# Performance work log

Measured on AMD Instinct MI355X. Metric: run time of the kernel, lower is better.

Reference implementation:

```python
import jax, jax.numpy as jnp
import numpy as np

V = 50257; E = 1024; H = 1024; L = 256; NL = 2; D = 10


def setup_inputs() -> dict:
    key = jax.random.key(0)
    ks = jax.random.split(key, 16)
    n = lambda k, s: jax.random.normal(k, s, dtype=jnp.float32)
    return {
        "input_tok": jax.random.randint(ks[0], (1, 1), 0, V),
        "h0": n(ks[1], (NL, 1, H)),
        "c0": n(ks[2], (NL, 1, H)),
        "h_s": n(ks[3], (L, 1, H)),
        "h_t_tilde": n(ks[4], (1, 1, H)),
        "emb": n(ks[5], (V, E)) * 0.02,
        "Wp": n(ks[6], (H, H)) * (H ** -0.5),
        "wdot": n(ks[7], (1, H)) * (H ** -0.5),
        "Wbil": n(ks[8], (1, H, H)) * (H ** -0.5),
        "Wcomb": n(ks[9], (H, 2 * H)) * ((2 * H) ** -0.5),
        "bcomb": jnp.zeros((H,), jnp.float32),
        "Wih0": n(ks[10], (4 * H, E + H)) * ((E + H) ** -0.5),
        "Whh0": n(ks[11], (4 * H, H)) * (H ** -0.5),
        "bih0": jnp.zeros((4 * H,), jnp.float32),
        "bhh0": jnp.zeros((4 * H,), jnp.float32),
        "Wih1": n(ks[12], (4 * H, H)) * (H ** -0.5),
        "Whh1": n(ks[13], (4 * H, H)) * (H ** -0.5),
        "bih1": jnp.zeros((4 * H,), jnp.float32),
        "bhh1": jnp.zeros((4 * H,), jnp.float32),
        "Wout": n(ks[14], (V, H)) * (H ** -0.5),
        "bout": jnp.zeros((V,), jnp.float32),
    }


def _lstm_cell(x, h, c, Wih, Whh, bih, bhh):
    # torch LSTM gate order: i, f, g, o
    g = x @ Wih.T + bih + h @ Whh.T + bhh
    i, f, gg, o = jnp.split(g, 4, axis=-1)
    c2 = jax.nn.sigmoid(f) * c + jax.nn.sigmoid(i) * jnp.tanh(gg)
    h2 = jax.nn.sigmoid(o) * jnp.tanh(c2)
    return h2, c2


def reference(input_tok, h0, c0, h_s, h_t_tilde, emb, Wp, wdot, Wbil, Wcomb, bcomb,
              Wih0, Whh0, bih0, bhh0, Wih1, Whh1, bih1, bhh1, Wout, bout):
    embedding = emb[input_tok]                                  # [1,1,E]
    x = jnp.concatenate((embedding, h_t_tilde), axis=-1)[0]     # [1,E+H]
    h1, c1 = _lstm_cell(x, h0[0], c0[0], Wih0, Whh0, bih0, bhh0)
    h2, c2 = _lstm_cell(h1, h0[1], c0[1], Wih1, Whh1, bih1, bhh1)
    h_new = jnp.stack((h1, h2)); c_new = jnp.stack((c1, c2))
    h_t = h2                                                    # [1,H]
    Ls = h_s.shape[0]
    p_t = Ls * jax.nn.sigmoid(jnp.tanh(h_t @ Wp.T) @ wdot.T).squeeze()  # scalar
    s = jnp.round(p_t).astype(jnp.int32)
    idx = jnp.arange(Ls)
    lo = jnp.maximum(s - D, 0); hi = jnp.minimum(s + D, Ls - 1)
    mask = (idx >= lo) & (idx <= hi)                            # [L] local window
    # bilinear score h_t^T W h_s over all positions; mask outside window
    score = jnp.einsum('bh,ohk,lbk->lbo', h_t, Wbil, h_s)       # [L,1,1]
    neg = jnp.finfo(score.dtype).min
    a = jax.nn.softmax(jnp.where(mask[:, None, None], score, neg), axis=0)
    # NOTE: original uses exp(+d^2/(D/2)^2) (no minus sign); replicated faithfully.
    expo = jnp.where(mask, ((idx.astype(jnp.float32) - p_t) ** 2) / ((D / 2) ** 2), 0.0)
    a_t = a * jnp.exp(expo)[:, None, None]                      # [L,1,1]
    win = (hi - lo + 1).astype(jnp.float32)
    context = jnp.sum(a_t * h_s, axis=0, keepdims=True) / win   # [1,1,H] (mean over window)
    cat = jnp.concatenate((context, h_t[None]), axis=-1)        # [1,1,2H]
    h_t_tilde_new = jnp.tanh(cat @ Wcomb.T + bcomb)             # [1,1,H]
    y = jax.nn.log_softmax(h_t_tilde_new @ Wout.T + bout, axis=-1)  # [1,1,V]
    return (y, h_new, c_new, h_t_tilde_new, a_t, p_t)
```

## Files before the change

### kernel.cpp

```cpp
#include <hip/hip_runtime.h>
#include <math.h>

#define V 50257
#define E 1024
#define HH 1024
#define LL 256

#define O_H  (V)
#define O_C  (V + 2*HH)
#define O_HT (V + 4*HH)
#define O_A  (V + 5*HH)
#define O_P  (V + 5*HH + LL)

#define W_T    0
#define W_V    1024
#define W_H1   2048
#define W_H2   3072
#define W_Z    4096
#define W_BM   54400
#define W_BS   55424

#define NW   4096
#define MAXR 13

__device__ __forceinline__ float sigmoidf_(float x) { return 1.f / (1.f + expf(-x)); }
__device__ __forceinline__ float dot4(float4 a, float4 b) {
    return a.x * b.x + a.y * b.y + a.z * b.z + a.w * b.w;
}

__device__ __forceinline__ float block_sum(float v, float* red) {
    int lane = threadIdx.x & 63, wv = threadIdx.x >> 6;
#pragma unroll
    for (int o = 32; o > 0; o >>= 1) v += __shfl_down(v, o, 64);
    __syncthreads();
    if (lane == 0) red[wv] = v;
    __syncthreads();
    return red[0] + red[1] + red[2] + red[3];
}

__global__ void k_lstm(const float* __restrict__ Wih, const float* __restrict__ Whh,
                       const float* __restrict__ bih, const float* __restrict__ bhh,
                       const float* __restrict__ xa_base, const int* __restrict__ tok,
                       const float* __restrict__ xb, int na, int nb,
                       const float* __restrict__ hprev, const float* __restrict__ cprev,
                       float* __restrict__ hout, float* __restrict__ cout,
                       float* __restrict__ hout2, float* __restrict__ zero_buf) {
    const int u = blockIdx.x;
    const int K = na + nb;
    const int K4 = K >> 2, na4 = na >> 2;
    if (zero_buf && threadIdx.x == 0) zero_buf[u] = 0.f;
    const float* xa = tok ? (xa_base + (size_t)tok[0] * na) : xa_base;
    const float4* xa4 = (const float4*)xa;
    const float4* xb4 = (const float4*)xb;
    const float4* r0 = (const float4*)(Wih + (size_t)u * K);
    const float4* r1 = (const float4*)(Wih + (size_t)(u + HH) * K);
    const float4* r2 = (const float4*)(Wih + (size_t)(u + 2*HH) * K);
    const float4* r3 = (const float4*)(Wih + (size_t)(u + 3*HH) * K);
    float a0 = 0, a1 = 0, a2 = 0, a3 = 0;
    for (int j = threadIdx.x; j < K4; j += 256) {
        float4 xv = (j < na4) ? xa4[j] : xb4[j - na4];
        a0 += dot4(r0[j], xv); a1 += dot4(r1[j], xv);
        a2 += dot4(r2[j], xv); a3 += dot4(r3[j], xv);
    }
    const float4* s0 = (const float4*)(Whh + (size_t)u * HH);
    const float4* s1 = (const float4*)(Whh + (size_t)(u + HH) * HH);
    const float4* s2 = (const float4*)(Whh + (size_t)(u + 2*HH) * HH);
    const float4* s3 = (const float4*)(Whh + (size_t)(u + 3*HH) * HH);
    const float4* hp4 = (const float4*)hprev;
    {
        int j = threadIdx.x;
        float4 hv = hp4[j];
        a0 += dot4(s0[j], hv); a1 += dot4(s1[j], hv);
        a2 += dot4(s2[j], hv); a3 += dot4(s3[j], hv);
    }
    int lane = threadIdx.x & 63, wv = threadIdx.x >> 6;
#pragma unroll
    for (int o = 32; o > 0; o >>= 1) {
        a0 += __shfl_down(a0, o, 64);
        a1 += __shfl_down(a1, o, 64);
        a2 += __shfl_down(a2, o, 64);
        a3 += __shfl_down(a3, o, 64);
    }
    __shared__ float sm[4][4];
    if (lane == 0) { sm[wv][0] = a0; sm[wv][1] = a1; sm[wv][2] = a2; sm[wv][3] = a3; }
    __syncthreads();
    if (threadIdx.x == 0) {
        float gi = sm[0][0]+sm[1][0]+sm[2][0]+sm[3][0] + bih[u]        + bhh[u];
        float gf = sm[0][1]+sm[1][1]+sm[2][1]+sm[3][1] + bih[u+HH]     + bhh[u+HH];
        float gg = sm[0][2]+sm[1][2]+sm[2][2]+sm[3][2] + bih[u+2*HH]   + bhh[u+2*HH];
        float go = sm[0][3]+sm[1][3]+sm[2][3]+sm[3][3] + bih[u+3*HH]   + bhh[u+3*HH];
        float c = sigmoidf_(gf) * cprev[u] + sigmoidf_(gi) * tanhf(gg);
        float h = sigmoidf_(go) * tanhf(c);
        hout[u] = h; cout[u] = c; hout2[u] = h;
    }
}

__global__ void k_ptv(const float* __restrict__ Wp, const float* __restrict__ Wbil,
                      const float* __restrict__ h2, float* __restrict__ t_out,
                      float* __restrict__ v_out) {
    __shared__ float red[4];
    if (blockIdx.x < HH) {
        int r = blockIdx.x;
        const float4* row = (const float4*)(Wp + (size_t)r * HH);
        const float4* h24 = (const float4*)h2;
        float acc = dot4(row[threadIdx.x], h24[threadIdx.x]);
        float tot = block_sum(acc, red);
        if (threadIdx.x == 0) t_out[r] = tanhf(tot);
    } else {
        int b = blockIdx.x - HH;
        int h0 = b * 32;
        int k4 = threadIdx.x;
        const float4* W4 = (const float4*)Wbil;
        float4 acc = make_float4(0.f, 0.f, 0.f, 0.f);
        for (int h = h0; h < h0 + 32; ++h) {
            float hv = h2[h];
            float4 w = W4[(size_t)h * 256 + k4];
            acc.x += hv * w.x; acc.y += hv * w.y;
            acc.z += hv * w.z; acc.w += hv * w.w;
        }
        atomicAdd(&v_out[k4 * 4 + 0], acc.x);
        atomicAdd(&v_out[k4 * 4 + 1], acc.y);
        atomicAdd(&v_out[k4 * 4 + 2], acc.z);
        atomicAdd(&v_out[k4 * 4 + 3], acc.w);
    }
}

__global__ void k_combattn(const float* __restrict__ wdot, const float* __restrict__ t,
                           const float* __restrict__ v, const float* __restrict__ hs,
                           const float* __restrict__ h2, const float* __restrict__ Wcomb,
                           const float* __restrict__ bcomb,
                           float* __restrict__ outv, float* __restrict__ outv2,
                           float* __restrict__ ato, float* __restrict__ pto) {
    const int u = blockIdx.x, tid = threadIdx.x;
    const int lane = tid & 63, wv = tid >> 6;
    __shared__ float red[4];
    __shared__ float ssc[32];
    __shared__ float sa[LL];
    float p;
    {
        const float4* w4 = (const float4*)wdot;
        const float4* t4 = (const float4*)t;
        float acc = dot4(w4[tid], t4[tid]);
        p = (float)LL * sigmoidf_(block_sum(acc, red));
    }
    if (u == 0 && tid == 0) pto[0] = p;
    const int si = (int)rintf(p);
    const int lo = max(si - 10, 0), hi = min(si + 10, LL - 1);
    const int W = hi - lo + 1;
    const float4* v4 = (const float4*)v;
    for (int l = lo + wv; l <= hi; l += 4) {
        const float4* row = (const float4*)(hs + (size_t)l * HH);
        float a = 0.f;
#pragma unroll
        for (int j = lane; j < 256; j += 64) a += dot4(row[j], v4[j]);
#pragma unroll
        for (int o = 32; o > 0; o >>= 1) a += __shfl_xor(a, o, 64);
        if (lane == 0) ssc[l - lo] = a;
    }
    __syncthreads();
    float M = -INFINITY;
    for (int i = 0; i < W; ++i) M = fmaxf(M, ssc[i]);
    float S = 0.f;
    for (int i = 0; i < W; ++i) S += expf(ssc[i] - M);
    {
        bool mask = (tid >= lo) && (tid <= hi);
        int wi = min(max(tid - lo, 0), 31);
        float e = mask ? expf(ssc[wi] - M) : 0.f;
        float d = (float)tid - p;
        float at = mask ? (e / S) * expf(d * d * 0.04f) : 0.f;
        sa[tid] = at;
        if (u == 0) ato[tid] = at;
    }
    __syncthreads();
    const float4* hs4 = (const float4*)hs;
    float4 c = make_float4(0.f, 0.f, 0.f, 0.f);
    for (int l = lo; l <= hi; ++l) {
        float a = sa[l];
        float4 hv = hs4[(size_t)l * 256 + tid];
        c.x += a * hv.x; c.y += a * hv.y; c.z += a * hv.z; c.w += a * hv.w;
    }
    const float inv_win = 1.f / (float)W;
    c.x *= inv_win; c.y *= inv_win; c.z *= inv_win; c.w *= inv_win;
    {
        const float4* row = (const float4*)(Wcomb + (size_t)u * (2 * HH));
        const float4* h24 = (const float4*)h2;
        float acc = dot4(row[tid], c) + dot4(row[256 + tid], h24[tid]);
        float tot = block_sum(acc, red);
        if (tid == 0) {
            float h = tanhf(tot + bcomb[u]);
            outv[u] = h; outv2[u] = h;
        }
    }
}

__global__ void k_logits(const float* __restrict__ Wout, const float* __restrict__ bout,
                         const float* __restrict__ x, float* __restrict__ z,
                         float* __restrict__ bmax, float* __restrict__ bsum) {
    const int tid = threadIdx.x, lane = tid & 63, wvi = tid >> 6;
    const int w = blockIdx.x * 4 + wvi;
    const float4* x4 = (const float4*)x;
    float4 x0 = x4[lane], x1 = x4[lane + 64], x2 = x4[lane + 128], x3 = x4[lane + 192];
    float m = -INFINITY, s = 0.f;
    for (int i = 0; i < MAXR; ++i) {
        int r = w + i * NW;
        if (r < V) {
            const float4* row = (const float4*)(Wout + (size_t)r * 1024) + lane;
            float acc = dot4(row[0], x0) + dot4(row[64], x1)
                      + dot4(row[128], x2) + dot4(row[192], x3);
#pragma unroll
            for (int o = 32; o > 0; o >>= 1) acc += __shfl_xor(acc, o, 64);
            float zz = acc + bout[r];
            if (lane == 0) z[r] = zz;
            if (zz > m) { s *= expf(m - zz); m = zz; }
            s += expf(zz - m);
        }
    }
    __shared__ float wm[4], wsv[4];
    if (lane == 0) { wm[wvi] = m; wsv[wvi] = s; }
    __syncthreads();
    if (tid == 0) {
        float M = fmaxf(fmaxf(wm[0], wm[1]), fmaxf(wm[2], wm[3]));
        float S = 0.f;
        if (M != -INFINITY) {
#pragma unroll
            for (int q = 0; q < 4; ++q)
                if (wm[q] != -INFINITY) S += wsv[q] * expf(wm[q] - M);
        }
        bmax[blockIdx.x] = M; bsum[blockIdx.x] = S;
    }
}

__global__ void k_sub(const float* __restrict__ z, const float* __restrict__ bmax,
                      const float* __restrict__ bsum, float* __restrict__ y) {
    int tid = threadIdx.x;
    float m = -INFINITY, s = 0.f;
    for (int i = tid; i < 1024; i += 256) {
        float m2 = bmax[i], s2 = bsum[i];
        float M = fmaxf(m, m2);
        if (M != -INFINITY) s = s * expf(m - M) + s2 * expf(m2 - M);
        m = M;
    }
    int lane = tid & 63, wv = tid >> 6;
#pragma unroll
    for (int o = 32; o > 0; o >>= 1) {
        float m2 = __shfl_down(m, o, 64), s2 = __shfl_down(s, o, 64);
        float M = fmaxf(m, m2);
        if (M != -INFINITY) s = s * expf(m - M) + s2 * expf(m2 - M);
        else s = 0.f;
        m = M;
    }
    __shared__ float wm[4], wsv[4];
    __shared__ float lzs;
    if (lane == 0) { wm[wv] = m; wsv[wv] = s; }
    __syncthreads();
    if (tid == 0) {
        float M = -INFINITY, S = 0.f;
#pragma unroll
        for (int q = 0; q < 4; ++q) {
            float M2 = fmaxf(M, wm[q]);
            if (M2 != -INFINITY) S = S * expf(M - M2) + wsv[q] * expf(wm[q] - M2);
            M = M2;
        }
        lzs = M + logf(S);
    }
    __syncthreads();
    float lz = lzs;
    int i = blockIdx.x * 256 + tid;
    if (i < V) y[i] = z[i] - lz;
}

extern "C" void kernel_launch(void* const* d_in, const int* in_sizes, int n_in,
                              void* d_out, int out_size, void* d_ws, size_t ws_size,
                              hipStream_t stream) {
    const int*   tok   = (const int*)  d_in[0];
    const float* h0    = (const float*)d_in[1];
    const float* c0    = (const float*)d_in[2];
    const float* hs    = (const float*)d_in[3];
    const float* htt   = (const float*)d_in[4];
    const float* emb   = (const float*)d_in[5];
    const float* Wp    = (const float*)d_in[6];
    const float* wdot  = (const float*)d_in[7];
    const float* Wbil  = (const float*)d_in[8];
    const float* Wcomb = (const float*)d_in[9];
    const float* bcomb = (const float*)d_in[10];
    const float* Wih0  = (const float*)d_in[11];
    const float* Whh0  = (const float*)d_in[12];
    const float* bih0  = (const float*)d_in[13];
    const float* bhh0  = (const float*)d_in[14];
    const float* Wih1  = (const float*)d_in[15];
    const float* Whh1  = (const float*)d_in[16];
    const float* bih1  = (const float*)d_in[17];
    const float* bhh1  = (const float*)d_in[18];
    const float* Wout  = (const float*)d_in[19];
    const float* bout  = (const float*)d_in[20];

    float* out = (float*)d_out;
    float* ws  = (float*)d_ws;

    float* h1o  = out + O_H;
    float* h2o  = out + O_H + HH;
    float* c1o  = out + O_C;
    float* c2o  = out + O_C + HH;
    float* htto = out + O_HT;
    float* ato  = out + O_A;
    float* pto  = out + O_P;

    hipLaunchKernelGGL(k_lstm, dim3(1024), dim3(256), 0, stream,
                       Wih0, Whh0, bih0, bhh0, emb, tok, htt, 1024, 1024,
                       h0, c0, h1o, c1o, ws + W_H1, ws + W_V);
    hipLaunchKernelGGL(k_lstm, dim3(1024), dim3(256), 0, stream,
                       Wih1, Whh1, bih1, bhh1, ws + W_H1, (const int*)nullptr,
                       ws + W_H1, 1024, 0,
                       h0 + HH, c0 + HH, h2o, c2o, ws + W_H2, (float*)nullptr);
    hipLaunchKernelGGL(k_ptv, dim3(1024 + 32), dim3(256), 0, stream,
                       Wp, Wbil, ws + W_H2, ws + W_T, ws + W_V);
    hipLaunchKernelGGL(k_combattn, dim3(1024), dim3(256), 0, stream,
                       wdot, ws + W_T, ws + W_V, hs, ws + W_H2, Wcomb, bcomb,
                       htto, ws + W_H1, ato, pto);
    hipLaunchKernelGGL(k_logits, dim3(1024), dim3(256), 0, stream,
                       Wout, bout, ws + W_H1, ws + W_Z, ws + W_BM, ws + W_BS);
    hipLaunchKernelGGL(k_sub, dim3((V + 255) / 256), dim3(256), 0, stream,
                       ws + W_Z, ws + W_BM, ws + W_BS, out);
}
```

Baseline: 86.27 us.

## Hoist layer-1 recurrent matvec into layer-0 kernel and widen logits blocks

The layer-1 Whh·h0[1] product depends only on the inputs, so it is now computed in the first LSTM kernel alongside layer 0, using 512-thread blocks. Its partial sums are stashed in the start of the output buffer, where y is later overwritten. The second LSTM kernel then only reads Wih1, which shortens the serial dependency chain. The logits kernel moves to 8 waves per block with 8192 rows per sweep, which raises occupancy and the number of loads in flight over the large Wout read.

```diff
diff --git a/kernel.cpp b/kernel.cpp
--- a/kernel.cpp
+++ b/kernel.cpp
@@ -20,8 +20,8 @@
 #define W_BM   54400
 #define W_BS   55424
 
-#define NW   4096
-#define MAXR 13
+#define NWL   8192
+#define MAXR  7
 
 __device__ __forceinline__ float sigmoidf_(float x) { return 1.f / (1.f + expf(-x)); }
 __device__ __forceinline__ float dot4(float4 a, float4 b) {
@@ -38,60 +38,108 @@
     return red[0] + red[1] + red[2] + red[3];
 }
 
-__global__ void k_lstm(const float* __restrict__ Wih, const float* __restrict__ Whh,
-                       const float* __restrict__ bih, const float* __restrict__ bhh,
-                       const float* __restrict__ xa_base, const int* __restrict__ tok,
-                       const float* __restrict__ xb, int na, int nb,
-                       const float* __restrict__ hprev, const float* __restrict__ cprev,
-                       float* __restrict__ hout, float* __restrict__ cout,
-                       float* __restrict__ hout2, float* __restrict__ zero_buf) {
-    const int u = blockIdx.x;
-    const int K = na + nb;
-    const int K4 = K >> 2, na4 = na >> 2;
-    if (zero_buf && threadIdx.x == 0) zero_buf[u] = 0.f;
-    const float* xa = tok ? (xa_base + (size_t)tok[0] * na) : xa_base;
-    const float4* xa4 = (const float4*)xa;
-    const float4* xb4 = (const float4*)xb;
-    const float4* r0 = (const float4*)(Wih + (size_t)u * K);
-    const float4* r1 = (const float4*)(Wih + (size_t)(u + HH) * K);
-    const float4* r2 = (const float4*)(Wih + (size_t)(u + 2*HH) * K);
-    const float4* r3 = (const float4*)(Wih + (size_t)(u + 3*HH) * K);
-    float a0 = 0, a1 = 0, a2 = 0, a3 = 0;
-    for (int j = threadIdx.x; j < K4; j += 256) {
-        float4 xv = (j < na4) ? xa4[j] : xb4[j - na4];
-        a0 += dot4(r0[j], xv); a1 += dot4(r1[j], xv);
-        a2 += dot4(r2[j], xv); a3 += dot4(r3[j], xv);
-    }
-    const float4* s0 = (const float4*)(Whh + (size_t)u * HH);
-    const float4* s1 = (const float4*)(Whh + (size_t)(u + HH) * HH);
-    const float4* s2 = (const float4*)(Whh + (size_t)(u + 2*HH) * HH);
-    const float4* s3 = (const float4*)(Whh + (size_t)(u + 3*HH) * HH);
-    const float4* hp4 = (const float4*)hprev;
-    {
-        int j = threadIdx.x;
-        float4 hv = hp4[j];
-        a0 += dot4(s0[j], hv); a1 += dot4(s1[j], hv);
-        a2 += dot4(s2[j], hv); a3 += dot4(s3[j], hv);
-    }
-    int lane = threadIdx.x & 63, wv = threadIdx.x >> 6;
+__global__ __launch_bounds__(512) void k_lstmA(
+    const float* __restrict__ Wih0, const float* __restrict__ Whh0,
+    const float* __restrict__ Whh1,
+    const float* __restrict__ bih0, const float* __restrict__ bhh0,
+    const float* __restrict__ emb, const int* __restrict__ tok,
+    const float* __restrict__ htt,
+    const float* __restrict__ h0, const float* __restrict__ c0,
+    float* __restrict__ h1o, float* __restrict__ c1o, float* __restrict__ h1w,
+    float* __restrict__ p1, float* __restrict__ vzero) {
+    const int u = blockIdx.x, tid = threadIdx.x;
+    if (tid == 0) vzero[u] = 0.f;
+    const float4* xa4 = (const float4*)(emb + (size_t)tok[0] * E);
+    const float4* xb4 = (const float4*)htt;
+    const float4* r0 = (const float4*)(Wih0 + (size_t)u * 2048);
+    const float4* r1 = (const float4*)(Wih0 + (size_t)(u + HH) * 2048);
+    const float4* r2 = (const float4*)(Wih0 + (size_t)(u + 2*HH) * 2048);
+    const float4* r3 = (const float4*)(Wih0 + (size_t)(u + 3*HH) * 2048);
+    float4 xv = (tid < 256) ? xa4[tid] : xb4[tid - 256];
+    float a0 = dot4(r0[tid], xv), a1 = dot4(r1[tid], xv);
+    float a2 = dot4(r2[tid], xv), a3 = dot4(r3[tid], xv);
+    float b0 = 0.f, b1 = 0.f, b2 = 0.f, b3 = 0.f;
+    if (tid < 256) {
+        const float4* s0 = (const float4*)(Whh0 + (size_t)u * HH);
+        const float4* s1 = (const float4*)(Whh0 + (size_t)(u + HH) * HH);
+        const float4* s2 = (const float4*)(Whh0 + (size_t)(u + 2*HH) * HH);
+        const float4* s3 = (const float4*)(Whh0 + (size_t)(u + 3*HH) * HH);
+        float4 hv = ((const float4*)h0)[tid];
+        a0 += dot4(s0[tid], hv); a1 += dot4(s1[tid], hv);
+        a2 += dot4(s2[tid], hv); a3 += dot4(s3[tid], hv);
+    } else {
+        int j = tid - 256;
+        const float4* t0 = (const float4*)(Whh1 + (size_t)u * HH);
+        const float4* t1 = (const float4*)(Whh1 + (size_t)(u + HH) * HH);
+        const float4* t2 = (const float4*)(Whh1 + (size_t)(u + 2*HH) * HH);
+        const float4* t3 = (const float4*)(Whh1 + (size_t)(u + 3*HH) * HH);
+        float4 gv = ((const float4*)(h0 + HH))[j];
+        b0 = dot4(t0[j], gv); b1 = dot4(t1[j], gv);
+        b2 = dot4(t2[j], gv); b3 = dot4(t3[j], gv);
+    }
+    const int lane = tid & 63, wv = tid >> 6;
 #pragma unroll
     for (int o = 32; o > 0; o >>= 1) {
-        a0 += __shfl_down(a0, o, 64);
-        a1 += __shfl_down(a1, o, 64);
-        a2 += __shfl_down(a2, o, 64);
-        a3 += __shfl_down(a3, o, 64);
+        a0 += __shfl_down(a0, o, 64); a1 += __shfl_down(a1, o, 64);
+        a2 += __shfl_down(a2, o, 64); a3 += __shfl_down(a3, o, 64);
+        b0 += __shfl_down(b0, o, 64); b1 += __shfl_down(b1, o, 64);
+        b2 += __shfl_down(b2, o, 64); b3 += __shfl_down(b3, o, 64);
+    }
+    __shared__ float sma[8][4], smb[8][4];
+    if (lane == 0) {
+        sma[wv][0] = a0; sma[wv][1] = a1; sma[wv][2] = a2; sma[wv][3] = a3;
+        smb[wv][0] = b0; smb[wv][1] = b1; smb[wv][2] = b2; smb[wv][3] = b3;
+    }
+    __syncthreads();
+    if (tid == 0) {
+        float g[4], p[4];
+#pragma unroll
+        for (int i = 0; i < 4; ++i) {
+            float ga = 0.f, pb = 0.f;
+#pragma unroll
+            for (int w = 0; w < 8; ++w) { ga += sma[w][i]; pb += smb[w][i]; }
+            g[i] = ga + bih0[u + i*HH] + bhh0[u + i*HH];
+            p[i] = pb;
+        }
+        float c = sigmoidf_(g[1]) * c0[u] + sigmoidf_(g[0]) * tanhf(g[2]);
+        float h = sigmoidf_(g[3]) * tanhf(c);
+        h1o[u] = h; c1o[u] = c; h1w[u] = h;
+        p1[u*4+0] = p[0]; p1[u*4+1] = p[1]; p1[u*4+2] = p[2]; p1[u*4+3] = p[3];
+    }
+}
+
+__global__ void k_lstmB(
+    const float* __restrict__ Wih1,
+    const float* __restrict__ bih1, const float* __restrict__ bhh1,
+    const float* __restrict__ h1w, const float* __restrict__ p1,
+    const float* __restrict__ h0, const float* __restrict__ c0,
+    float* __restrict__ h2o, float* __restrict__ c2o, float* __restrict__ h2w) {
+    const int u = blockIdx.x, tid = threadIdx.x;
+    const float4* r0 = (const float4*)(Wih1 + (size_t)u * HH);
+    const float4* r1 = (const float4*)(Wih1 + (size_t)(u + HH) * HH);
+    const float4* r2 = (const float4*)(Wih1 + (size_t)(u + 2*HH) * HH);
+    const float4* r3 = (const float4*)(Wih1 + (size_t)(u + 3*HH) * HH);
+    float4 hv = ((const float4*)h1w)[tid];
+    float a0 = dot4(r0[tid], hv), a1 = dot4(r1[tid], hv);
+    float a2 = dot4(r2[tid], hv), a3 = dot4(r3[tid], hv);
+    const int lane = tid & 63, wv = tid >> 6;
+#pragma unroll
+    for (int o = 32; o > 0; o >>= 1) {
+        a0 += __shfl_down(a0, o, 64); a1 += __shfl_down(a1, o, 64);
+        a2 += __shfl_down(a2, o, 64); a3 += __shfl_down(a3, o, 64);
     }
     __shared__ float sm[4][4];
     if (lane == 0) { sm[wv][0] = a0; sm[wv][1] = a1; sm[wv][2] = a2; sm[wv][3] = a3; }
     __syncthreads();
-    if (threadIdx.x == 0) {
-        float gi = sm[0][0]+sm[1][0]+sm[2][0]+sm[3][0] + bih[u]        + bhh[u];
-        float gf = sm[0][1]+sm[1][1]+sm[2][1]+sm[3][1] + bih[u+HH]     + bhh[u+HH];
-        float gg = sm[0][2]+sm[1][2]+sm[2][2]+sm[3][2] + bih[u+2*HH]   + bhh[u+2*HH];
-        float go = sm[0][3]+sm[1][3]+sm[2][3]+sm[3][3] + bih[u+3*HH]   + bhh[u+3*HH];
-        float c = sigmoidf_(gf) * cprev[u] + sigmoidf_(gi) * tanhf(gg);
-        float h = sigmoidf_(go) * tanhf(c);
-        hout[u] = h; cout[u] = c; hout2[u] = h;
+    if (tid == 0) {
+        float g[4];
+#pragma unroll
+        for (int i = 0; i < 4; ++i)
+            g[i] = sm[0][i] + sm[1][i] + sm[2][i] + sm[3][i]
+                 + p1[u*4+i] + bih1[u + i*HH] + bhh1[u + i*HH];
+        float c = sigmoidf_(g[1]) * c0[HH + u] + sigmoidf_(g[0]) * tanhf(g[2]);
+        float h = sigmoidf_(g[3]) * tanhf(c);
+        h2o[u] = h; c2o[u] = c; h2w[u] = h;
     }
 }
 
@@ -193,16 +241,17 @@
     }
 }
 
-__global__ void k_logits(const float* __restrict__ Wout, const float* __restrict__ bout,
-                         const float* __restrict__ x, float* __restrict__ z,
-                         float* __restrict__ bmax, float* __restrict__ bsum) {
+__global__ __launch_bounds__(512) void k_logits(
+    const float* __restrict__ Wout, const float* __restrict__ bout,
+    const float* __restrict__ x, float* __restrict__ z,
+    float* __restrict__ bmax, float* __restrict__ bsum) {
     const int tid = threadIdx.x, lane = tid & 63, wvi = tid >> 6;
-    const int w = blockIdx.x * 4 + wvi;
+    const int w = blockIdx.x * 8 + wvi;
     const float4* x4 = (const float4*)x;
     float4 x0 = x4[lane], x1 = x4[lane + 64], x2 = x4[lane + 128], x3 = x4[lane + 192];
     float m = -INFINITY, s = 0.f;
     for (int i = 0; i < MAXR; ++i) {
-        int r = w + i * NW;
+        int r = w + i * NWL;
         if (r < V) {
             const float4* row = (const float4*)(Wout + (size_t)r * 1024) + lane;
             float acc = dot4(row[0], x0) + dot4(row[64], x1)
@@ -215,15 +264,17 @@
             s += expf(zz - m);
         }
     }
-    __shared__ float wm[4], wsv[4];
+    __shared__ float wm[8], wsv[8];
     if (lane == 0) { wm[wvi] = m; wsv[wvi] = s; }
     __syncthreads();
     if (tid == 0) {
-        float M = fmaxf(fmaxf(wm[0], wm[1]), fmaxf(wm[2], wm[3]));
+        float M = -INFINITY;
+#pragma unroll
+        for (int q = 0; q < 8; ++q) M = fmaxf(M, wm[q]);
         float S = 0.f;
         if (M != -INFINITY) {
 #pragma unroll
-            for (int q = 0; q < 4; ++q)
+            for (int q = 0; q < 8; ++q)
                 if (wm[q] != -INFINITY) S += wsv[q] * expf(wm[q] - M);
         }
         bmax[blockIdx.x] = M; bsum[blockIdx.x] = S;
@@ -304,20 +355,20 @@
     float* htto = out + O_HT;
     float* ato  = out + O_A;
     float* pto  = out + O_P;
-
-    hipLaunchKernelGGL(k_lstm, dim3(1024), dim3(256), 0, stream,
-                       Wih0, Whh0, bih0, bhh0, emb, tok, htt, 1024, 1024,
-                       h0, c0, h1o, c1o, ws + W_H1, ws + W_V);
-    hipLaunchKernelGGL(k_lstm, dim3(1024), dim3(256), 0, stream,
-                       Wih1, Whh1, bih1, bhh1, ws + W_H1, (const int*)nullptr,
-                       ws + W_H1, 1024, 0,
-                       h0 + HH, c0 + HH, h2o, c2o, ws + W_H2, (float*)nullptr);
+    float* p1   = out;
+
+    hipLaunchKernelGGL(k_lstmA, dim3(1024), dim3(512), 0, stream,
+                       Wih0, Whh0, Whh1, bih0, bhh0, emb, tok, htt, h0, c0,
+                       h1o, c1o, ws + W_H1, p1, ws + W_V);
+    hipLaunchKernelGGL(k_lstmB, dim3(1024), dim3(256), 0, stream,
+                       Wih1, bih1, bhh1, ws + W_H1, p1, h0, c0,
+                       h2o, c2o, ws + W_H2);
     hipLaunchKernelGGL(k_ptv, dim3(1024 + 32), dim3(256), 0, stream,
                        Wp, Wbil, ws + W_H2, ws + W_T, ws + W_V);
     hipLaunchKernelGGL(k_combattn, dim3(1024), dim3(256), 0, stream,
                        wdot, ws + W_T, ws + W_V, hs, ws + W_H2, Wcomb, bcomb,
                        htto, ws + W_H1, ato, pto);
-    hipLaunchKernelGGL(k_logits, dim3(1024), dim3(256), 0, stream,
+    hipLaunchKernelGGL(k_logits, dim3(1024), dim3(512), 0, stream,
                        Wout, bout, ws + W_H1, ws + W_Z, ws + W_BM, ws + W_BS);
     hipLaunchKernelGGL(k_sub, dim3((V + 255) / 256), dim3(256), 0, stream,
                        ws + W_Z, ws + W_BM, ws + W_BS, out);
```

After: 84.92 us. Within noise of the previous version (-1.6%).
